# Kernel tuning notes

Measured on AMD Instinct MI355X. Metric: run time of the kernel, lower is better.

## Reference

```python
import jax, jax.numpy as jnp
import numpy as np

K = 32
TEMP = 0.01
OTHERWEIGHT = 0.5
BS = 64
F = 128


def setup_inputs() -> dict:
    key = jax.random.key(0)
    k1, k2, k3 = jax.random.split(key, 3)
    feats1 = jax.random.normal(k1, (K * BS, F), dtype=jnp.float32)
    feats2 = jax.random.normal(k2, (K * BS, F), dtype=jnp.float32)
    overlap_inds = jax.random.randint(k3, (K,), 0, 2).astype(bool)
    return {"feats1": feats1, "feats2": feats2, "overlap_inds": overlap_inds, "bs": BS}


def _labels(overlap_inds, bs):
    k = overlap_inds.shape[0]
    labels1 = jnp.repeat(jnp.arange(k), bs)
    nov = (~overlap_inds).astype(jnp.int32)
    excl_nov = jnp.cumsum(nov) - nov  # exclusive count of non-overlaps before i
    class2 = jnp.where(overlap_inds, jnp.arange(k), k + excl_nov)
    labels2 = jnp.repeat(class2, bs)
    return jnp.concatenate([labels1, labels2])


def reference(feats1, feats2, overlap_inds, bs):
    n1 = feats1.shape[0]
    labels = _labels(overlap_inds, bs)            # [n]
    feats = jnp.concatenate([feats1, feats2])     # [n, F]
    n = feats.shape[0]

    logits = (feats @ feats.T) * TEMP             # [n, n]; log of exp(sim*temp)
    sim = jnp.exp(logits)

    same = labels[:, None] == labels[None, :]
    eye = jnp.eye(n, dtype=bool)
    pos_mask = same & ~eye
    neg_mask = ~same

    is2 = jnp.arange(n) >= n1                     # second-view block indicator
    cross_w = jnp.where(is2[:, None] != is2[None, :], OTHERWEIGHT, 1.0)

    neg_sum = jnp.sum(jnp.where(neg_mask, sim, 0.0), axis=1)      # [n]
    # -log(pos / neg_sum) = log(neg_sum) - logits
    per_pair_loss = cross_w * (jnp.log(neg_sum)[:, None] - logits)
    total_loss = jnp.sum(jnp.where(pos_mask, per_pair_loss, 0.0))
    total_pos = jnp.sum(pos_mask)

    # accuracy: a positive pair counts iff its sim beats ALL negatives in its row
    max_neg = jnp.max(jnp.where(neg_mask, sim, -jnp.inf), axis=1)  # [n]
    correct = pos_mask & (sim > max_neg[:, None])
    acc = jnp.sum(correct).astype(jnp.float32) / total_pos.astype(jnp.float32)

    loss = total_loss / total_pos.astype(jnp.float32)
    return acc, loss
```

## Files before the change

### kernel.cpp

```cpp
#include <hip/hip_runtime.h>
#include <math.h>

#define TEMP 0.01f

typedef __attribute__((ext_vector_type(8))) short short8;
typedef __attribute__((ext_vector_type(4))) float f32x4;
typedef __attribute__((ext_vector_type(8))) unsigned short ushort8_t;


__device__ __forceinline__ unsigned bf16_hi_bits(float x) {
  unsigned u = __float_as_uint(x);
  return (u + 0x7FFFu + ((u >> 16) & 1u)) >> 16;
}

struct HL { unsigned short h, l; };

__device__ __forceinline__ HL split1(float x) {
  unsigned hb = bf16_hi_bits(x);
  float hf = __uint_as_float(hb << 16);
  unsigned lb = bf16_hi_bits(x - hf);
  HL r;
  r.h = (unsigned short)hb;
  r.l = (unsigned short)lb;
  return r;
}

__device__ __forceinline__ void decode_ov(const int* __restrict__ ov_raw,
                                          int* s_class2, int* s_v2b,
                                          int* s_ov) {
  const int t = threadIdx.x;
  if (t < 64) {
    int v = (t < 32) ? ov_raw[t] : 0;
    bool valid = (t >= 32) || (v == 0) || (v == 1);
    unsigned long long okmask = __ballot(valid);
    bool as_int = (okmask == ~0ull);
    s_v2b[t] = 0;
    if (t < 32) {
      int o = as_int ? v : (((const unsigned char*)ov_raw)[t] ? 1 : 0);
      s_ov[t] = o;
      unsigned long long nz = __ballot((t < 32) && !o);
      int cum = __popcll(nz & ((1ull << t) - 1ull));
      int c2 = o ? t : 32 + cum;
      s_class2[t] = c2;
      s_v2b[c2] = t;
    }
  }
}

__device__ __forceinline__ int labf(int g, const int* s_class2) {
  return (g < 2048) ? (g >> 6) : s_class2[(g - 2048) >> 6];
}

__device__ __forceinline__ int slotf(int g, int cls, const int* s_v2b) {
  if (g < 2048) return g - (cls << 6);
  return ((cls < 32) ? 64 : 0) + (g - 2048 - (s_v2b[cls] << 6));
}

__global__ __launch_bounds__(256) void precompute_kernel(
    const float* __restrict__ f1, const float* __restrict__ f2,
    unsigned short* __restrict__ Ph, unsigned short* __restrict__ Pl,
    float* __restrict__ accum, int* __restrict__ counter) {
  if (blockIdx.x == 0 && threadIdx.x == 0) {
    accum[0] = 0.f; accum[1] = 0.f; accum[2] = 0.f; *counter = 0;
  }
  const int u = blockIdx.x * 256 + threadIdx.x;
  const int row = u >> 4;
  const int gid = u & 15;
  const int kc = gid >> 3, P = gid & 7;
  const int k = kc * 64 + (P ^ (row & 7)) * 8;
  const float* src = (row < 2048) ? (f1 + (size_t)row * 128)
                                  : (f2 + (size_t)(row - 2048) * 128);
  const float4 a = *(const float4*)(src + k);
  const float4 b = *(const float4*)(src + k + 4);
  ushort8_t hi, lo;
  HL s;
  s = split1(a.x); hi.s0 = s.h; lo.s0 = s.l;
  s = split1(a.y); hi.s1 = s.h; lo.s1 = s.l;
  s = split1(a.z); hi.s2 = s.h; lo.s2 = s.l;
  s = split1(a.w); hi.s3 = s.h; lo.s3 = s.l;
  s = split1(b.x); hi.s4 = s.h; lo.s4 = s.l;
  s = split1(b.y); hi.s5 = s.h; lo.s5 = s.l;
  s = split1(b.z); hi.s6 = s.h; lo.s6 = s.l;
  s = split1(b.w); hi.s7 = s.h; lo.s7 = s.l;
  *(ushort8_t*)&Ph[(size_t)row * 128 + gid * 8] = hi;
  *(ushort8_t*)&Pl[(size_t)row * 128 + gid * 8] = lo;
}

__device__ __forceinline__ void compute_tile(
    int bi, int bj, bool diag,
    const unsigned short* __restrict__ Ph, const unsigned short* __restrict__ Pl,
    unsigned short (*Ah)[64], unsigned short (*Al)[64],
    unsigned short (*Bh)[64], unsigned short (*Bl)[64],
    const int* s_class2, const int* s_v2b,
    float4* __restrict__ P4, float* __restrict__ posbuf) {
  const int ibase = bi * 128, jbase = bj * 128;
  const int t = threadIdx.x;
  const int l = t & 63;
  const int wid = t >> 6;
  const int wy = wid >> 1, wx = wid & 1;
  const int rr = l & 15;
  const int q = l >> 4;
  const int sw = l & 7;

  f32x4 acc[4][4];
#pragma unroll
  for (int mi = 0; mi < 4; ++mi)
#pragma unroll
    for (int ni = 0; ni < 4; ++ni) acc[mi][ni] = (f32x4)0.0f;

  const int gg = t & 7;
  const int r0 = t >> 3;

  for (int kc = 0; kc < 2; ++kc) {
    __syncthreads();
#pragma unroll
    for (int p = 0; p < 4; ++p) {
      const int r = r0 + 32 * p;
      const size_t arec = (size_t)(ibase + r) * 128 + kc * 64 + gg * 8;
      const ushort8_t vah = *(const ushort8_t*)&Ph[arec];
      const ushort8_t val = *(const ushort8_t*)&Pl[arec];
      *(ushort8_t*)&Ah[r][gg * 8] = vah;
      *(ushort8_t*)&Al[r][gg * 8] = val;
      if (!diag) {
        const size_t brec = (size_t)(jbase + r) * 128 + kc * 64 + gg * 8;
        const ushort8_t vbh = *(const ushort8_t*)&Ph[brec];
        const ushort8_t vbl = *(const ushort8_t*)&Pl[brec];
        *(ushort8_t*)&Bh[r][gg * 8] = vbh;
        *(ushort8_t*)&Bl[r][gg * 8] = vbl;
      }
    }
    __syncthreads();

#pragma unroll
    for (int s = 0; s < 2; ++s) {
      const int pb = ((((s << 2) | q)) ^ sw) << 3;
      short8 afh[4], afl[4], bfh[4], bfl[4];
#pragma unroll
      for (int mi = 0; mi < 4; ++mi) {
        const int ar = wy * 64 + mi * 16 + rr;
        afh[mi] = *(const short8*)&Ah[ar][pb];
        afl[mi] = *(const short8*)&Al[ar][pb];
        const int br = wx * 64 + mi * 16 + rr;
        bfh[mi] = diag ? *(const short8*)&Ah[br][pb]
                       : *(const short8*)&Bh[br][pb];
        bfl[mi] = diag ? *(const short8*)&Al[br][pb]
                       : *(const short8*)&Bl[br][pb];
      }
#pragma unroll
      for (int mi = 0; mi < 4; ++mi)
#pragma unroll
        for (int ni = 0; ni < 4; ++ni) {
          acc[mi][ni] = __builtin_amdgcn_mfma_f32_16x16x32_bf16(
              afh[mi], bfh[ni], acc[mi][ni], 0, 0, 0);
          acc[mi][ni] = __builtin_amdgcn_mfma_f32_16x16x32_bf16(
              afh[mi], bfl[ni], acc[mi][ni], 0, 0, 0);
          acc[mi][ni] = __builtin_amdgcn_mfma_f32_16x16x32_bf16(
              afl[mi], bfh[ni], acc[mi][ni], 0, 0, 0);
        }
    }
  }

  const bool off = !diag;
  const float cw = ((ibase < 2048) != (jbase < 2048)) ? 0.5f : 1.0f;
  int gj[4], lj[4];
#pragma unroll
  for (int ni = 0; ni < 4; ++ni) {
    gj[ni] = jbase + wx * 64 + ni * 16 + rr;
    lj[ni] = labf(gj[ni], s_class2);
  }

  float cnsum[4], cnmax[4], cpcw[4], cpcwl[4];
#pragma unroll
  for (int ni = 0; ni < 4; ++ni) {
    cnsum[ni] = 0.f; cnmax[ni] = 0.f; cpcw[ni] = 0.f; cpcwl[ni] = 0.f;
  }

#pragma unroll
  for (int mi = 0; mi < 4; ++mi) {
#pragma unroll
    for (int reg = 0; reg < 4; ++reg) {
      const int gi = ibase + wy * 64 + mi * 16 + q * 4 + reg;
      const int li = labf(gi, s_class2);
      float rnsum = 0.f, rnmax = 0.f, rpcw = 0.f, rpcwl = 0.f;
#pragma unroll
      for (int ni = 0; ni < 4; ++ni) {
        const int gjj = gj[ni];
        if (gi == gjj) continue;
        const float logit = acc[mi][ni][reg] * TEMP;
        const float e = __expf(logit);
        if (li == lj[ni]) {
          rpcw += cw;
          rpcwl += cw * logit;
          posbuf[(size_t)gi * 128 + slotf(gjj, li, s_v2b)] = e;
          if (off) {
            cpcw[ni] += cw;
            cpcwl[ni] += cw * logit;
            posbuf[(size_t)gjj * 128 + slotf(gi, li, s_v2b)] = e;
          }
        } else {
          rnsum += e;
          rnmax = fmaxf(rnmax, e);
          if (off) {
            cnsum[ni] += e;
            cnmax[ni] = fmaxf(cnmax[ni], e);
          }
        }
      }
#pragma unroll
      for (int m = 1; m < 16; m <<= 1) {
        rnsum += __shfl_xor(rnsum, m, 64);
        rpcw  += __shfl_xor(rpcw, m, 64);
        rpcwl += __shfl_xor(rpcwl, m, 64);
        rnmax = fmaxf(rnmax, __shfl_xor(rnmax, m, 64));
      }
      if (rr == 0) {
        float4 v; v.x = rnsum; v.y = rpcw; v.z = rpcwl; v.w = rnmax;
        P4[(size_t)gi * 64 + (bj * 2 + wx)] = v;
      }
    }
  }

  if (off) {
#pragma unroll
    for (int ni = 0; ni < 4; ++ni) {
      float cs = cnsum[ni], cm = cnmax[ni], cp = cpcw[ni], cl = cpcwl[ni];
#pragma unroll
      for (int m = 16; m < 64; m <<= 1) {
        cs += __shfl_xor(cs, m, 64);
        cp += __shfl_xor(cp, m, 64);
        cl += __shfl_xor(cl, m, 64);
        cm = fmaxf(cm, __shfl_xor(cm, m, 64));
      }
      if (q == 0) {
        float4 v; v.x = cs; v.y = cp; v.z = cl; v.w = cm;
        P4[(size_t)gj[ni] * 64 + (bi * 2 + wy)] = v;
      }
    }
  }
}

__global__ __launch_bounds__(256, 2) void main_kernel(
    const unsigned short* __restrict__ Ph, const unsigned short* __restrict__ Pl,
    const int* __restrict__ ov_raw, float4* __restrict__ P4,
    float* __restrict__ posbuf) {
  __shared__ unsigned short Ah[128][64], Al[128][64];
  __shared__ unsigned short Bh[128][64], Bl[128][64];
  __shared__ int s_class2[32], s_v2b[64], s_ov[32];

  decode_ov(ov_raw, s_class2, s_v2b, s_ov);

  const int bid = blockIdx.x;
  if (bid < 496) {
    int idx = bid, bi = 0;
    while (idx >= 31 - bi) { idx -= 31 - bi; ++bi; }
    const int bj = bi + 1 + idx;
    compute_tile(bi, bj, false, Ph, Pl, Ah, Al, Bh, Bl, s_class2, s_v2b, P4,
                 posbuf);
  } else {
    const int d = (bid - 496) * 2;
    compute_tile(d, d, true, Ph, Pl, Ah, Al, Bh, Bl, s_class2, s_v2b, P4,
                 posbuf);
    compute_tile(d + 1, d + 1, true, Ph, Pl, Ah, Al, Bh, Bl, s_class2, s_v2b,
                 P4, posbuf);
  }
}

__global__ __launch_bounds__(256) void finalize_kernel(
    const int* __restrict__ ov_raw, const float4* __restrict__ P4,
    const float* __restrict__ posbuf, float* __restrict__ accum,
    int* __restrict__ counter, float* __restrict__ out) {
  __shared__ int s_class2[32], s_v2b[64], s_ov[32];
  __shared__ float sc[4], sp[4], sl[4];
  decode_ov(ov_raw, s_class2, s_v2b, s_ov);
  __syncthreads();

  const int t = threadIdx.x;
  const int w = t >> 6, lane = t & 63;
  float cnt_acc = 0.f, pos_acc = 0.f, loss_acc = 0.f;
  const int rbase = blockIdx.x * 16 + w * 4;
  for (int i = 0; i < 4; ++i) {
    const int row = rbase + i;
    float4 p = P4[(size_t)row * 64 + lane];
#pragma unroll
    for (int m = 1; m < 64; m <<= 1) {
      p.x += __shfl_xor(p.x, m, 64);
      p.y += __shfl_xor(p.y, m, 64);
      p.z += __shfl_xor(p.z, m, 64);
      p.w = fmaxf(p.w, __shfl_xor(p.w, m, 64));
    }
    const float nmax = p.w;
    const float2 pv = *(const float2*)&posbuf[(size_t)row * 128 + lane * 2];
    const int c = labf(row, s_class2);
    const int size = (c < 32) ? (s_ov[c] ? 128 : 64) : 64;
    int selfslot;
    if (row < 2048) selfslot = row - (c << 6);
    else selfslot = ((c < 32) ? 64 : 0) + (row - 2048 - (s_v2b[c] << 6));
    const int s0 = lane * 2;
    int h = 0;
    if (s0 < size && s0 != selfslot && pv.x > nmax) h++;
    if (s0 + 1 < size && s0 + 1 != selfslot && pv.y > nmax) h++;
    cnt_acc += (float)h;
    if (lane == 0) {
      loss_acc += logf(p.x) * p.y - p.z;
      pos_acc += (float)(size - 1);
    }
  }
#pragma unroll
  for (int m = 1; m < 64; m <<= 1) {
    cnt_acc += __shfl_xor(cnt_acc, m, 64);
    pos_acc += __shfl_xor(pos_acc, m, 64);
    loss_acc += __shfl_xor(loss_acc, m, 64);
  }
  if (lane == 0) { sc[w] = cnt_acc; sp[w] = pos_acc; sl[w] = loss_acc; }
  __syncthreads();
  if (t == 0) {
    atomicAdd(&accum[0], sc[0] + sc[1] + sc[2] + sc[3]);
    atomicAdd(&accum[1], sp[0] + sp[1] + sp[2] + sp[3]);
    atomicAdd(&accum[2], sl[0] + sl[1] + sl[2] + sl[3]);
    __threadfence();
    const int prev = atomicAdd(counter, 1);
    if (prev == 255) {
      const float c = atomicAdd(&accum[0], 0.0f);
      const float tp = atomicAdd(&accum[1], 0.0f);
      const float lo = atomicAdd(&accum[2], 0.0f);
      out[0] = c / tp;
      out[1] = lo / tp;
    }
  }
}

extern "C" void kernel_launch(void* const* d_in, const int* in_sizes, int n_in,
                              void* d_out, int out_size, void* d_ws,
                              size_t ws_size, hipStream_t stream) {
  const float* f1 = (const float*)d_in[0];
  const float* f2 = (const float*)d_in[1];
  const int* ov = (const int*)d_in[2];
  float* out = (float*)d_out;

  float* wsf = (float*)d_ws;
  int* wsi = (int*)d_ws;
  float* accum  = wsf;
  int* counter  = wsi + 3;
  float* posbuf = wsf + 16;
  float4* P4    = (float4*)(wsf + 524304);
  unsigned short* Ph = (unsigned short*)(wsf + 1572880);
  unsigned short* Pl = Ph + 524288;

  precompute_kernel<<<256, 256, 0, stream>>>(f1, f2, Ph, Pl, accum, counter);
  main_kernel<<<512, 256, 0, stream>>>(Ph, Pl, ov, P4, posbuf);
  finalize_kernel<<<256, 256, 0, stream>>>(ov, P4, posbuf, accum, counter,
                                           out);
}
```

Before: 110.9 us.

## Reduce epilogue partials through shared memory instead of wave shuffles

The per-row and per-column partial reductions (negative sum, positive logit sum, negative max) are no longer done with cross-lane shuffles. Each lane now writes its raw partials into reused LDS tile buffers, and after a barrier threads sum them with vectorized loads before writing P4. The positive-weight count is dropped from the partials and recomputed analytically in the final kernel (95 or 63 per row), which also trims one shuffle chain there. This removes many shuffle instructions but adds two block barriers and LDS traffic, and the analytic count depends on the fixed class-size structure.

```diff
diff --git a/kernel.cpp b/kernel.cpp
--- a/kernel.cpp
+++ b/kernel.cpp
@@ -162,6 +162,14 @@
 
   const bool off = !diag;
   const float cw = ((ibase < 2048) != (jbase < 2048)) ? 0.5f : 1.0f;
+
+  float* RowPn = (float*)&Ah[0][0];
+  float* RowPl = (float*)&Al[0][0];
+  float* RowPm = (float*)&Bh[0][0];
+  float* ColPn = (float*)&Bl[0][0];
+  float* ColPl = ColPn + 1024;
+  float* ColPm = ColPn + 2048;
+
   int gj[4], lj[4];
 #pragma unroll
   for (int ni = 0; ni < 4; ++ni) {
@@ -169,11 +177,13 @@
     lj[ni] = labf(gj[ni], s_class2);
   }
 
-  float cnsum[4], cnmax[4], cpcw[4], cpcwl[4];
+  float cnsum[4], cnmax[4], clsum[4];
 #pragma unroll
   for (int ni = 0; ni < 4; ++ni) {
-    cnsum[ni] = 0.f; cnmax[ni] = 0.f; cpcw[ni] = 0.f; cpcwl[ni] = 0.f;
-  }
+    cnsum[ni] = 0.f; cnmax[ni] = 0.f; clsum[ni] = 0.f;
+  }
+
+  __syncthreads();
 
 #pragma unroll
   for (int mi = 0; mi < 4; ++mi) {
@@ -181,7 +191,7 @@
     for (int reg = 0; reg < 4; ++reg) {
       const int gi = ibase + wy * 64 + mi * 16 + q * 4 + reg;
       const int li = labf(gi, s_class2);
-      float rnsum = 0.f, rnmax = 0.f, rpcw = 0.f, rpcwl = 0.f;
+      float rn = 0.f, rl = 0.f, rm = 0.f;
 #pragma unroll
       for (int ni = 0; ni < 4; ++ni) {
         const int gjj = gj[ni];
@@ -189,53 +199,72 @@
         const float logit = acc[mi][ni][reg] * TEMP;
         const float e = __expf(logit);
         if (li == lj[ni]) {
-          rpcw += cw;
-          rpcwl += cw * logit;
+          rl += logit;
           posbuf[(size_t)gi * 128 + slotf(gjj, li, s_v2b)] = e;
           if (off) {
-            cpcw[ni] += cw;
-            cpcwl[ni] += cw * logit;
+            clsum[ni] += logit;
             posbuf[(size_t)gjj * 128 + slotf(gi, li, s_v2b)] = e;
           }
         } else {
-          rnsum += e;
-          rnmax = fmaxf(rnmax, e);
+          rn += e;
+          rm = fmaxf(rm, e);
           if (off) {
             cnsum[ni] += e;
             cnmax[ni] = fmaxf(cnmax[ni], e);
           }
         }
       }
-#pragma unroll
-      for (int m = 1; m < 16; m <<= 1) {
-        rnsum += __shfl_xor(rnsum, m, 64);
-        rpcw  += __shfl_xor(rpcw, m, 64);
-        rpcwl += __shfl_xor(rpcwl, m, 64);
-        rnmax = fmaxf(rnmax, __shfl_xor(rnmax, m, 64));
-      }
-      if (rr == 0) {
-        float4 v; v.x = rnsum; v.y = rpcw; v.z = rpcwl; v.w = rnmax;
-        P4[(size_t)gi * 64 + (bj * 2 + wx)] = v;
-      }
-    }
-  }
-
+      const int widx = ((mi * 4 + reg) * 4 + wid) * 64 + l;
+      RowPn[widx] = rn;
+      RowPl[widx] = rl;
+      RowPm[widx] = rm;
+    }
+  }
   if (off) {
 #pragma unroll
     for (int ni = 0; ni < 4; ++ni) {
-      float cs = cnsum[ni], cm = cnmax[ni], cp = cpcw[ni], cl = cpcwl[ni];
-#pragma unroll
-      for (int m = 16; m < 64; m <<= 1) {
-        cs += __shfl_xor(cs, m, 64);
-        cp += __shfl_xor(cp, m, 64);
-        cl += __shfl_xor(cl, m, 64);
-        cm = fmaxf(cm, __shfl_xor(cm, m, 64));
-      }
-      if (q == 0) {
-        float4 v; v.x = cs; v.y = cp; v.z = cl; v.w = cm;
-        P4[(size_t)gj[ni] * 64 + (bi * 2 + wy)] = v;
-      }
-    }
+      const int widx = (ni * 4 + wid) * 64 + l;
+      ColPn[widx] = cnsum[ni];
+      ColPl[widx] = clsum[ni];
+      ColPm[widx] = cnmax[ni];
+    }
+  }
+  __syncthreads();
+
+  {
+    const int r = t >> 1, h = t & 1;
+    const int g = (((r >> 4) & 3) * 4) + (r & 3);
+    const int w2 = (r >> 6) * 2 + h;
+    const int base = (g * 4 + w2) * 64 + ((r >> 2) & 3) * 16;
+    const float4* pn = (const float4*)&RowPn[base];
+    const float4* pl = (const float4*)&RowPl[base];
+    const float4* pm = (const float4*)&RowPm[base];
+    float ns = 0.f, ls = 0.f, nm = 0.f;
+#pragma unroll
+    for (int i = 0; i < 4; ++i) {
+      const float4 a = pn[i], b = pl[i], c = pm[i];
+      ns += a.x + a.y + a.z + a.w;
+      ls += b.x + b.y + b.z + b.w;
+      nm = fmaxf(nm, fmaxf(fmaxf(c.x, c.y), fmaxf(c.z, c.w)));
+    }
+    float4 v; v.x = ns; v.y = 0.f; v.z = cw * ls; v.w = nm;
+    P4[(size_t)(ibase + r) * 64 + (bj * 2 + h)] = v;
+  }
+
+  if (off) {
+    const int c = t >> 1, hy = t & 1;
+    const int w2 = hy * 2 + (c >> 6);
+    const int base = (((c >> 4) & 3) * 4 + w2) * 64 + (c & 15);
+    float ns = 0.f, ls = 0.f, nm = 0.f;
+#pragma unroll
+    for (int q4 = 0; q4 < 4; ++q4) {
+      const int idx = base + q4 * 16;
+      ns += ColPn[idx];
+      ls += ColPl[idx];
+      nm = fmaxf(nm, ColPm[idx]);
+    }
+    float4 v; v.x = ns; v.y = 0.f; v.z = cw * ls; v.w = nm;
+    P4[(size_t)(jbase + c) * 64 + (bi * 2 + hy)] = v;
   }
 }
 
@@ -284,14 +313,14 @@
 #pragma unroll
     for (int m = 1; m < 64; m <<= 1) {
       p.x += __shfl_xor(p.x, m, 64);
-      p.y += __shfl_xor(p.y, m, 64);
       p.z += __shfl_xor(p.z, m, 64);
       p.w = fmaxf(p.w, __shfl_xor(p.w, m, 64));
     }
     const float nmax = p.w;
     const float2 pv = *(const float2*)&posbuf[(size_t)row * 128 + lane * 2];
     const int c = labf(row, s_class2);
-    const int size = (c < 32) ? (s_ov[c] ? 128 : 64) : 64;
+    const bool both = (row < 2048) ? (s_ov[c] != 0) : (c < 32);
+    const int size = both ? 128 : 64;
     int selfslot;
     if (row < 2048) selfslot = row - (c << 6);
     else selfslot = ((c < 32) ? 64 : 0) + (row - 2048 - (s_v2b[c] << 6));
@@ -301,7 +330,8 @@
     if (s0 + 1 < size && s0 + 1 != selfslot && pv.y > nmax) h++;
     cnt_acc += (float)h;
     if (lane == 0) {
-      loss_acc += logf(p.x) * p.y - p.z;
+      const float pcw = both ? 95.f : 63.f;
+      loss_acc += logf(p.x) * pcw - p.z;
       pos_acc += (float)(size - 1);
     }
   }
```

New measurement: 106.4 us. 1.04x faster.
